# Optimization experiments

Hardware: AMD Instinct MI355X
Metric: run time of the kernel (lower is better)

## Reference

```python
import jax, jax.numpy as jnp
import numpy as np

EMBED_DIM = 1024
NUM_HEADS = 16
HEAD_DIM = EMBED_DIM // NUM_HEADS
SCALE = HEAD_DIM ** -0.5


def setup_inputs() -> dict:
    key = jax.random.key(0)
    k_x, k_qkv_w, k_qkv_b, k_p_w, k_p_b = jax.random.split(key, 5)
    B, N, C = 4, 2048, EMBED_DIM
    std = C ** -0.5
    return {
        "x": jax.random.normal(k_x, (B, N, C), dtype=jnp.float32),
        "qkv_w": jax.random.normal(k_qkv_w, (C, 3 * C), dtype=jnp.float32) * std,
        "qkv_b": jax.random.normal(k_qkv_b, (3 * C,), dtype=jnp.float32) * 0.02,
        "proj_w": jax.random.normal(k_p_w, (C, C), dtype=jnp.float32) * std,
        "proj_b": jax.random.normal(k_p_b, (C,), dtype=jnp.float32) * 0.02,
    }


def reference(x, qkv_w, qkv_b, proj_w, proj_b):
    B, N, C = x.shape
    H, D = NUM_HEADS, HEAD_DIM
    # fused QKV projection: [B, N, 3C] -> [3, B, H, N, D]
    qkv = (x @ qkv_w + qkv_b).reshape(B, N, 3, H, D).transpose(2, 0, 3, 1, 4)
    q, k, v = qkv[0], qkv[1], qkv[2]
    # explicit N x N attention (faithful to the original, no fused SDPA)
    attn = jnp.einsum("bhqd,bhkd->bhqk", q, k) * SCALE
    attn = jax.nn.softmax(attn, axis=-1)
    out = jnp.einsum("bhqk,bhkd->bhqd", attn, v)  # [B, H, N, D]
    out = out.transpose(0, 2, 1, 3).reshape(B, N, C)
    return out @ proj_w + proj_b
```

## Files before the change

kernel.cpp:

```cpp
#include <hip/hip_runtime.h>
#include <hip/hip_bf16.h>

typedef __bf16 bf16x8 __attribute__((ext_vector_type(8)));
typedef __bf16 bf16x4 __attribute__((ext_vector_type(4)));
typedef float  f32x4  __attribute__((ext_vector_type(4)));

#define MFMA_BF16(a, b, c) __builtin_amdgcn_mfma_f32_16x16x32_bf16((a), (b), (c), 0, 0, 0)

typedef const __attribute__((address_space(1))) void* gas_ptr;
typedef __attribute__((address_space(3))) void* las_ptr;

__device__ __forceinline__ void gload_lds16(const void* g, void* l) {
    __builtin_amdgcn_global_load_lds((gas_ptr)g, (las_ptr)l, 16, 0, 0);
}

__device__ __forceinline__ float fast_exp2(float x) {
#if __has_builtin(__builtin_amdgcn_exp2f)
    return __builtin_amdgcn_exp2f(x);
#else
    return __builtin_exp2f(x);
#endif
}

#define LOG2E 1.44269504088896f
#define QSCALE 0.1803368801111204f

__global__ __launch_bounds__(256) void cvt_f32_bf16(const float* __restrict__ in,
                                                    __bf16* __restrict__ out, int n4) {
    int i = blockIdx.x * 256 + threadIdx.x;
    if (i < n4) {
        float4 v = ((const float4*)in)[i];
        bf16x4 o = {(__bf16)v.x, (__bf16)v.y, (__bf16)v.z, (__bf16)v.w};
        ((bf16x4*)out)[i] = o;
    }
}

__global__ __launch_bounds__(256) void transpose_cvt(const float* __restrict__ in,
                                                     __bf16* __restrict__ out, int R, int C) {
    __shared__ float t[32][33];
    int bx = blockIdx.x * 32, by = blockIdx.y * 32;
    int x = bx + threadIdx.x;
    for (int j = threadIdx.y; j < 32; j += 8)
        t[j][threadIdx.x] = in[(size_t)(by + j) * C + x];
    __syncthreads();
    int x2 = by + threadIdx.x;
    for (int j = threadIdx.y; j < 32; j += 8)
        out[(size_t)(bx + j) * R + x2] = (__bf16)t[threadIdx.x][j];
}

template <int MODE>
__global__ __launch_bounds__(256) void gemm_bt(const __bf16* __restrict__ A,
                                               const __bf16* __restrict__ Bt,
                                               const float* __restrict__ bias,
                                               float* __restrict__ outp,
                                               __bf16* __restrict__ Qp,
                                               __bf16* __restrict__ Kp,
                                               __bf16* __restrict__ Vp,
                                               int M, int Nn, int K) {
    __shared__ __align__(16) __bf16 As[128 * 32];
    __shared__ __align__(16) __bf16 Bs[128 * 32];
    const int tid = threadIdx.x, lane = tid & 63, w = tid >> 6;
    const int wr = w >> 1, wc = w & 1;
    const int nbx = Nn >> 7;
    const int nwg = (M >> 7) * nbx;
    const int cpx = nwg >> 3;
    const int id = blockIdx.x;
    const int nid = (id & 7) * cpx + (id >> 3);
    const int row0 = (nid / nbx) * 128, col0 = (nid % nbx) * 128;
    const __bf16* Ag = A + (size_t)row0 * K;
    const __bf16* Bg = Bt + (size_t)col0 * K;
    const int lr = lane >> 2;
    const int lk = (lane & 3) * 8;
    const int frow = lane & 15, fq = lane >> 4;
    f32x4 acc[4][4];
    for (int i = 0; i < 4; ++i)
        for (int j = 0; j < 4; ++j) acc[i][j] = (f32x4)0.f;

    for (int k0 = 0; k0 < K; k0 += 32) {
        __syncthreads();
        for (int it = 0; it < 2; ++it) {
            int ci = 2 * w + it;
            gload_lds16(Ag + (size_t)(ci * 16 + lr) * K + k0 + lk, &As[ci * 512]);
            gload_lds16(Bg + (size_t)(ci * 16 + lr) * K + k0 + lk, &Bs[ci * 512]);
        }
        __syncthreads();
        bf16x8 af[4], bf[4];
        for (int i = 0; i < 4; ++i)
            af[i] = *(const bf16x8*)&As[(wr * 64 + i * 16 + frow) * 32 + fq * 8];
        for (int j = 0; j < 4; ++j)
            bf[j] = *(const bf16x8*)&Bs[(wc * 64 + j * 16 + frow) * 32 + fq * 8];
        for (int i = 0; i < 4; ++i)
            for (int j = 0; j < 4; ++j) acc[i][j] = MFMA_BF16(af[i], bf[j], acc[i][j]);
    }

    for (int i = 0; i < 4; ++i) {
        int rbase = row0 + wr * 64 + i * 16 + fq * 4;
        for (int j = 0; j < 4; ++j) {
            int c = col0 + wc * 64 + j * 16 + frow;
            float bv = bias[c];
            if (MODE == 0) {
                int which = c >> 10;
                int h = (c >> 6) & 15;
                int d = c & 63;
                if (which == 2) {
                    int b = rbase >> 11, n = rbase & 2047;
                    int nph = (n & ~31) | (((n >> 2) & 3) << 3) | (((n >> 4) & 1) << 2) |
                              (n & 3);
                    bf16x4 vv = {(__bf16)(acc[i][j][0] + bv), (__bf16)(acc[i][j][1] + bv),
                                 (__bf16)(acc[i][j][2] + bv), (__bf16)(acc[i][j][3] + bv)};
                    *(bf16x4*)&Vp[(size_t)(((b << 4) + h) * 64 + d) * 2048 + nph] = vv;
                } else {
                    for (int rg = 0; rg < 4; ++rg) {
                        int rr = rbase + rg;
                        int b = rr >> 11, n = rr & 2047;
                        float v = acc[i][j][rg] + bv;
                        if (which == 0)
                            Qp[(size_t)(((b << 4) + h) * 2048 + n) * 64 + d] =
                                (__bf16)(v * QSCALE);
                        else
                            Kp[(size_t)(((b << 4) + h) * 2048 + n) * 64 + d] = (__bf16)v;
                    }
                }
            } else {
                for (int rg = 0; rg < 4; ++rg)
                    outp[(size_t)(rbase + rg) * Nn + c] = acc[i][j][rg] + bv;
            }
        }
    }
}

__global__ __launch_bounds__(256, 4) void flash_attn7(const __bf16* __restrict__ Q,
                                                      const __bf16* __restrict__ K,
                                                      const __bf16* __restrict__ Vt,
                                                      __bf16* __restrict__ O) {
    __shared__ __align__(16) __bf16 Kts[2][4096];
    __shared__ __align__(16) __bf16 Vts[2][4096];
    const int tid = threadIdx.x, lane = tid & 63, w = tid >> 6;
    const int frow = lane & 15, fq = lane >> 4;
    const int id = blockIdx.x;
    const int nid = (id & 7) * 128 + (id >> 3);
    const int bh = nid >> 4;
    const int q0 = (nid & 15) * 128;
    const __bf16* Qg = Q + ((size_t)bh * 2048 + q0 + w * 32) * 64;
    const __bf16* Kb = K + (size_t)bh * 2048 * 64;
    const __bf16* Vb = Vt + (size_t)bh * 64 * 2048;

    bf16x8 qf[2][2];
#pragma unroll
    for (int nt = 0; nt < 2; ++nt)
#pragma unroll
        for (int ks = 0; ks < 2; ++ks)
            qf[nt][ks] = *(const bf16x8*)(Qg + (nt * 16 + frow) * 64 + ks * 32 + fq * 8);

    bf16x8 ones;
#pragma unroll
    for (int i = 0; i < 8; ++i) ones[i] = (__bf16)1.0f;

    f32x4 acc[2][4];
#pragma unroll
    for (int i = 0; i < 2; ++i)
#pragma unroll
        for (int j = 0; j < 4; ++j) acc[i][j] = (f32x4)0.f;
    f32x4 acc_l[2];
#pragma unroll
    for (int i = 0; i < 2; ++i) acc_l[i] = (f32x4)0.f;

    const int s_r16 = lane >> 2;
    const int s_c8 = (((lane & 3) ^ ((lane >> 3) & 3))) * 8;

    auto stage = [&](int kt, __bf16* Kd, __bf16* Vd) {
#pragma unroll
        for (int it = 0; it < 2; ++it) {
            int ci = 2 * w + it;
            int ks = ci >> 2;
            int r16 = (ci & 3) * 16 + s_r16;
            gload_lds16(Kb + (size_t)(kt * 64 + r16) * 64 + ks * 32 + s_c8, Kd + ci * 512);
            gload_lds16(Vb + (size_t)r16 * 2048 + kt * 64 + ks * 32 + s_c8, Vd + ci * 512);
        }
    };

    stage(0, Kts[0], Vts[0]);

    const int key = (frow >> 1) & 3;
    const int slot = (fq ^ key) * 8;

    auto body = [&](int kt, const __bf16* Kc, const __bf16* Vc, __bf16* Kn, __bf16* Vn) {
        __syncthreads();
        if (kt < 31) stage(kt + 1, Kn, Vn);

#pragma unroll
        for (int ph = 0; ph < 2; ++ph) {
            bf16x8 pf[2];
#pragma unroll
            for (int mi = 0; mi < 2; ++mi) {
                int mt = ph * 2 + mi;
                bf16x8 a0 = *(const bf16x8*)&Kc[(mt * 16 + frow) * 32 + slot];
                bf16x8 a1 = *(const bf16x8*)&Kc[2048 + (mt * 16 + frow) * 32 + slot];
#pragma unroll
                for (int nt = 0; nt < 2; ++nt) {
                    f32x4 s = MFMA_BF16(a0, qf[nt][0], (f32x4)0.f);
                    s = MFMA_BF16(a1, qf[nt][1], s);
                    pf[nt][mi * 4 + 0] = (__bf16)fast_exp2(s[0]);
                    pf[nt][mi * 4 + 1] = (__bf16)fast_exp2(s[1]);
                    pf[nt][mi * 4 + 2] = (__bf16)fast_exp2(s[2]);
                    pf[nt][mi * 4 + 3] = (__bf16)fast_exp2(s[3]);
                }
            }

            __builtin_amdgcn_s_setprio(1);
#pragma unroll
            for (int nt = 0; nt < 4; ++nt) {
                bf16x8 vf = *(const bf16x8*)&Vc[ph * 2048 + (nt * 16 + frow) * 32 + slot];
                acc[0][nt] = MFMA_BF16(pf[0], vf, acc[0][nt]);
                acc[1][nt] = MFMA_BF16(pf[1], vf, acc[1][nt]);
            }
            acc_l[0] = MFMA_BF16(pf[0], ones, acc_l[0]);
            acc_l[1] = MFMA_BF16(pf[1], ones, acc_l[1]);
            __builtin_amdgcn_s_setprio(0);
        }
    };

    for (int kt = 0; kt < 32; kt += 2) {
        body(kt, Kts[0], Vts[0], Kts[1], Vts[1]);
        body(kt + 1, Kts[1], Vts[1], Kts[0], Vts[0]);
    }

    const int b = bh >> 4, h = bh & 15;
#pragma unroll
    for (int mq = 0; mq < 2; ++mq)
#pragma unroll
        for (int r = 0; r < 4; ++r) {
            float linv = 1.0f / acc_l[mq][r];
            int qg = q0 + w * 32 + mq * 16 + fq * 4 + r;
            __bf16* orow = O + ((size_t)(b * 2048 + qg)) * 1024 + h * 64 + frow;
#pragma unroll
            for (int nt = 0; nt < 4; ++nt)
                orow[nt * 16] = (__bf16)(acc[mq][nt][r] * linv);
        }
}

extern "C" void kernel_launch(void* const* d_in, const int* in_sizes, int n_in,
                              void* d_out, int out_size, void* d_ws, size_t ws_size,
                              hipStream_t stream) {
    const float* x      = (const float*)d_in[0];
    const float* qkv_w  = (const float*)d_in[1];
    const float* qkv_b  = (const float*)d_in[2];
    const float* proj_w = (const float*)d_in[3];
    const float* proj_b = (const float*)d_in[4];
    float* out = (float*)d_out;

    char* ws = (char*)d_ws;
    __bf16* Xb     = (__bf16*)(ws);
    __bf16* Wqkvt  = (__bf16*)(ws + 16777216);
    __bf16* Wpt    = (__bf16*)(ws + 23068672);
    __bf16* Qb     = (__bf16*)(ws + 25165824);
    __bf16* Kb     = (__bf16*)(ws + 41943040);
    __bf16* Vtb    = (__bf16*)(ws + 58720256);
    __bf16* AttnOut = Xb;

    cvt_f32_bf16<<<8192, 256, 0, stream>>>(x, Xb, 2097152);
    transpose_cvt<<<dim3(96, 32), dim3(32, 8), 0, stream>>>(qkv_w, Wqkvt, 1024, 3072);
    transpose_cvt<<<dim3(32, 32), dim3(32, 8), 0, stream>>>(proj_w, Wpt, 1024, 1024);

    gemm_bt<0><<<1536, 256, 0, stream>>>(Xb, Wqkvt, qkv_b, nullptr,
                                         Qb, Kb, Vtb, 8192, 3072, 1024);

    flash_attn7<<<1024, 256, 0, stream>>>(Qb, Kb, Vtb, AttnOut);

    gemm_bt<1><<<512, 256, 0, stream>>>(AttnOut, Wpt, proj_b, out,
                                        nullptr, nullptr, nullptr, 8192, 1024, 1024);
}
```

Baseline: 271.4 us.

## Triple-buffer GEMM LDS tiles with async prefetch and XOR swizzle

Replaces the single-buffered LDS staging in the bf16 GEMM with a three-slot ring. Tiles t+1 and t+2 are in flight while tile t is computed, synchronised with vmcnt waits and a single barrier per iteration. It also XOR-swizzles the 16-byte chunk placement within each LDS row to reduce bank conflicts on fragment reads. The cost is triple the LDS footprint, which may reduce occupancy, and it relies on manual waitcnt counting being correct.

Measured after the change: 271.4 us. About the same (-0.0%).

```diff
diff --git a/kernel.cpp b/kernel.cpp
--- a/kernel.cpp
+++ b/kernel.cpp
@@ -57,8 +57,8 @@
                                                __bf16* __restrict__ Kp,
                                                __bf16* __restrict__ Vp,
                                                int M, int Nn, int K) {
-    __shared__ __align__(16) __bf16 As[128 * 32];
-    __shared__ __align__(16) __bf16 Bs[128 * 32];
+    __shared__ __align__(16) __bf16 SA[3][4096];
+    __shared__ __align__(16) __bf16 SB[3][4096];
     const int tid = threadIdx.x, lane = tid & 63, w = tid >> 6;
     const int wr = w >> 1, wc = w & 1;
     const int nbx = Nn >> 7;
@@ -70,27 +70,51 @@
     const __bf16* Ag = A + (size_t)row0 * K;
     const __bf16* Bg = Bt + (size_t)col0 * K;
     const int lr = lane >> 2;
-    const int lk = (lane & 3) * 8;
+    const int srcc = ((lane & 3) ^ ((lane >> 3) & 3)) * 8;
     const int frow = lane & 15, fq = lane >> 4;
+    const int rdoff = (fq ^ ((frow >> 1) & 3)) * 8;
     f32x4 acc[4][4];
     for (int i = 0; i < 4; ++i)
         for (int j = 0; j < 4; ++j) acc[i][j] = (f32x4)0.f;
 
-    for (int k0 = 0; k0 < K; k0 += 32) {
-        __syncthreads();
+    auto stage = [&](int t, __bf16* Ad, __bf16* Bd) {
+#pragma unroll
         for (int it = 0; it < 2; ++it) {
             int ci = 2 * w + it;
-            gload_lds16(Ag + (size_t)(ci * 16 + lr) * K + k0 + lk, &As[ci * 512]);
-            gload_lds16(Bg + (size_t)(ci * 16 + lr) * K + k0 + lk, &Bs[ci * 512]);
-        }
-        __syncthreads();
+            gload_lds16(Ag + (size_t)(ci * 16 + lr) * K + t * 32 + srcc, Ad + ci * 512);
+            gload_lds16(Bg + (size_t)(ci * 16 + lr) * K + t * 32 + srcc, Bd + ci * 512);
+        }
+    };
+
+    const int NK = K >> 5;
+    __bf16 *cA = SA[0], *cB = SB[0];
+    __bf16 *nA = SA[1], *nB = SB[1];
+    __bf16 *sA = SA[2], *sB = SB[2];
+    stage(0, cA, cB);
+    stage(1, nA, nB);
+
+    for (int t = 0; t < NK; ++t) {
+        if (t < NK - 1)
+            asm volatile("s_waitcnt vmcnt(4)" ::: "memory");
+        else
+            asm volatile("s_waitcnt vmcnt(0)" ::: "memory");
+        __builtin_amdgcn_s_barrier();
+        if (t + 2 < NK) stage(t + 2, sA, sB);
+
         bf16x8 af[4], bf[4];
+#pragma unroll
         for (int i = 0; i < 4; ++i)
-            af[i] = *(const bf16x8*)&As[(wr * 64 + i * 16 + frow) * 32 + fq * 8];
+            af[i] = *(const bf16x8*)&cA[(wr * 64 + i * 16 + frow) * 32 + rdoff];
+#pragma unroll
         for (int j = 0; j < 4; ++j)
-            bf[j] = *(const bf16x8*)&Bs[(wc * 64 + j * 16 + frow) * 32 + fq * 8];
+            bf[j] = *(const bf16x8*)&cB[(wc * 64 + j * 16 + frow) * 32 + rdoff];
+#pragma unroll
         for (int i = 0; i < 4; ++i)
+#pragma unroll
             for (int j = 0; j < 4; ++j) acc[i][j] = MFMA_BF16(af[i], bf[j], acc[i][j]);
+
+        __bf16* tA = cA; cA = nA; nA = sA; sA = tA;
+        __bf16* tB = cB; cB = nB; nB = sB; sB = tB;
     }
 
     for (int i = 0; i < 4; ++i) {
```
